# Optimization experiments

Measured on AMD Instinct MI355X. Metric: run time of the kernel, lower is better.

The kernel has to match this reference:

```python
import jax, jax.numpy as jnp
import numpy as np

L, D, N = 4096, 1024, 16  # seq_len, d_model, hiddens_per_input


def setup_inputs() -> dict:
    key = jax.random.key(0)
    ks = jax.random.split(key, 9)
    x = jax.random.normal(ks[0], (L, D), dtype=jnp.float32)
    # Delta param (pre-softplus); softplus(Delta) > 0 is the discretization step
    Delta = jax.random.normal(ks[1], (D,), dtype=jnp.float32)
    # A stored as (re, im); default scheme uses A_re = -1 (stable), theta in [0, 2pi)
    A_re = -(0.5 + 0.5 * jax.random.uniform(ks[2], (D, N), dtype=jnp.float32))
    A_im = jax.random.uniform(ks[3], (D, N), dtype=jnp.float32) * 2.0 * jnp.pi
    scale = 1.0 / jnp.sqrt(jnp.float32(D))  # matrix_init: randn / sqrt(shape[0])
    B_re = jax.random.normal(ks[4], (D, N), dtype=jnp.float32) * scale
    B_im = jax.random.normal(ks[5], (D, N), dtype=jnp.float32) * scale
    C_re = jax.random.normal(ks[6], (D, N), dtype=jnp.float32) * scale
    C_im = jax.random.normal(ks[7], (D, N), dtype=jnp.float32) * scale
    D_param = jax.random.normal(ks[8], (D,), dtype=jnp.float32) * scale
    return {"x": x, "Delta": Delta, "A_re": A_re, "A_im": A_im,
            "B_re": B_re, "B_im": B_im, "C_re": C_re, "C_im": C_im,
            "D_param": D_param}


def _binary_operator_diag(q_i, q_j):
    """Associative op for diagonal linear recurrence h_j = A_j h_{j-1} + b_j."""
    A_i, b_i = q_i
    A_j, b_j = q_j
    return (A_j * A_i, A_j * b_i + b_j)


def reference(x, Delta, A_re, A_im, B_re, B_im, C_re, C_im, D_param):
    Bc = B_re + 1j * B_im                      # (D, N) complex
    Cc = C_re + 1j * C_im                      # (D, N) complex
    Ac = A_re + 1j * A_im                      # (D, N) complex
    dt = jax.nn.softplus(Delta)                # (D,)
    # shared_Delta=True branch: Lambda = exp(dt[:, None] * A), repeated over L
    Lam = jnp.exp(dt[:, None] * Ac)            # (D, N) complex
    Lambda_elements = jnp.broadcast_to(Lam[None, :, :], (x.shape[0], *Lam.shape))
    # Bu = einsum('D, D N, L D -> L D N', dt, B, x)
    Bu_elements = jnp.einsum('D,DN,LD->LDN', dt.astype(Bc.dtype), Bc,
                             x.astype(Bc.dtype))
    _, hidden_states = jax.lax.associative_scan(
        _binary_operator_diag, (Lambda_elements, Bu_elements))  # (L, D, N)
    out = jnp.einsum('LDN,DN->LD', hidden_states, Cc) + D_param[None, :] * x
    return out.real
```

## Files before the change

kernel.cpp:

```cpp
#include <hip/hip_runtime.h>
#include <math.h>

constexpr int L  = 4096;
constexpr int D  = 1024;
constexpr int N  = 16;
constexpr int NC = 128;
constexpr int T  = L / NC;

__device__ __forceinline__ float softplus_f(float v) {
    return fmaxf(v, 0.0f) + log1pf(expf(-fabsf(v)));
}

__global__ __launch_bounds__(256) void k_pre(
    const float* __restrict__ Delta,
    const float* __restrict__ A_re, const float* __restrict__ A_im,
    const float* __restrict__ B_re, const float* __restrict__ B_im,
    const float* __restrict__ C_re, const float* __restrict__ C_im,
    float* __restrict__ PLr, float* __restrict__ PLi,
    float* __restrict__ PTr, float* __restrict__ PTi,
    float* __restrict__ PCr, float* __restrict__ PCi)
{
    const int tid = blockIdx.x * 256 + threadIdx.x;
    const int d = tid & (D - 1);
    const int n = tid >> 10;
    const int idx = d * N + n;

    const float dt = softplus_f(Delta[d]);
    float e  = expf(A_re[idx] * dt);
    float th = A_im[idx] * dt;
    float lr = e * cosf(th), li = e * sinf(th);
    float tr = lr, ti = li;
    #pragma unroll
    for (int k = 0; k < 5; ++k) {
        float nr = tr * tr - ti * ti;
        ti = 2.0f * tr * ti;
        tr = nr;
    }
    float br = B_re[idx], bi = B_im[idx];
    float cr = C_re[idx], ci = C_im[idx];
    PLr[tid] = lr; PLi[tid] = li;
    PTr[tid] = tr; PTi[tid] = ti;
    PCr[tid] = dt * (cr * br - ci * bi);
    PCi[tid] = dt * (cr * bi + ci * br);
}

__global__ __launch_bounds__(256, 4) void k_local(
    const float* __restrict__ x,
    const float* __restrict__ PLr, const float* __restrict__ PLi,
    float2* __restrict__ s2)
{
    __shared__ float xs[T * 64];
    const int bc = blockIdx.x >> 4;
    const int dg = blockIdx.x & 15;
    const int tid = threadIdx.x;

    const float* xg = x + (size_t)bc * T * D + dg * 64;
    #pragma unroll
    for (int it = 0; it < 2; ++it) {
        int f = tid * 4 + it * 1024;
        int row = f >> 6, col = f & 63;
        *(float4*)&xs[row * 64 + col] = *(const float4*)(xg + (size_t)row * D + col);
    }

    const int q = tid & 3, dl = tid >> 2;
    const int d = dg * 64 + dl;
    float Lr[4], Li[4];
    #pragma unroll
    for (int j = 0; j < 4; ++j) {
        int n = q * 4 + j;
        Lr[j] = PLr[n * D + d];
        Li[j] = PLi[n * D + d];
    }
    __syncthreads();

    float gr[4] = {0, 0, 0, 0}, gi[4] = {0, 0, 0, 0};
    #pragma unroll
    for (int i = 0; i < T; ++i) {
        float xv = xs[i * 64 + dl];
        #pragma unroll
        for (int j = 0; j < 4; ++j) {
            float t2 = fmaf(-Li[j], gi[j], xv);
            float nr = fmaf(Lr[j], gr[j], t2);
            gi[j] = fmaf(Lr[j], gi[j], Li[j] * gr[j]);
            gr[j] = nr;
        }
    }
    #pragma unroll
    for (int j = 0; j < 4; ++j) {
        int n = q * 4 + j;
        s2[((size_t)bc * N + n) * D + d] = make_float2(gr[j], gi[j]);
    }
}

__global__ __launch_bounds__(256) void k_scan(
    const float* __restrict__ PTr, const float* __restrict__ PTi,
    float2* __restrict__ s2)
{
    const int tid = blockIdx.x * 256 + threadIdx.x;
    const float Lr = PTr[tid], Li = PTi[tid];

    float cr = 0.0f, ci = 0.0f;
    for (int c0 = 0; c0 < NC; c0 += 16) {
        float2 sv[16];
        #pragma unroll
        for (int u = 0; u < 16; ++u)
            sv[u] = s2[(size_t)(c0 + u) * (N * D) + tid];
        #pragma unroll
        for (int u = 0; u < 16; ++u) {
            s2[(size_t)(c0 + u) * (N * D) + tid] = make_float2(cr, ci);
            float nr = fmaf(Lr, cr, fmaf(-Li, ci, sv[u].x));
            ci = fmaf(Lr, ci, fmaf(Li, cr, sv[u].y));
            cr = nr;
        }
    }
}

__global__ __launch_bounds__(256, 4) void k_out(
    const float* __restrict__ x,
    const float* __restrict__ PLr, const float* __restrict__ PLi,
    const float* __restrict__ PCr, const float* __restrict__ PCi,
    const float* __restrict__ Dp,
    const float2* __restrict__ s2,
    float* __restrict__ out)
{
    __shared__ float xs[T * 64];
    const int bc = blockIdx.x >> 4;
    const int dg = blockIdx.x & 15;
    const int tid = threadIdx.x;

    const float* xg = x + (size_t)bc * T * D + dg * 64;
    #pragma unroll
    for (int it = 0; it < 2; ++it) {
        int f = tid * 4 + it * 1024;
        int row = f >> 6, col = f & 63;
        *(float4*)&xs[row * 64 + col] = *(const float4*)(xg + (size_t)row * D + col);
    }

    const int q = tid & 3, dl = tid >> 2;
    const int d = dg * 64 + dl;
    float Lr[4], Li[4], Cr[4], Ci[4], gr[4], gi[4];
    #pragma unroll
    for (int j = 0; j < 4; ++j) {
        int n = q * 4 + j;
        Lr[j] = PLr[n * D + d];
        Li[j] = PLi[n * D + d];
        Cr[j] = PCr[n * D + d];
        Ci[j] = PCi[n * D + d];
        float2 cv = s2[((size_t)bc * N + n) * D + d];
        gr[j] = cv.x; gi[j] = cv.y;
    }
    const float dpv = Dp[d];
    float* og = out + (size_t)bc * T * D + dg * 64;
    __syncthreads();

    #pragma unroll
    for (int ib = 0; ib < T / 4; ++ib) {
        float keep = 0.0f;
        #pragma unroll
        for (int u = 0; u < 4; ++u) {
            int i = ib * 4 + u;
            float xv = xs[i * 64 + dl];
            float acc = 0.0f;
            #pragma unroll
            for (int j = 0; j < 4; ++j) {
                float t2 = fmaf(-Li[j], gi[j], xv);
                float nr = fmaf(Lr[j], gr[j], t2);
                gi[j] = fmaf(Lr[j], gi[j], Li[j] * gr[j]);
                gr[j] = nr;
                acc = fmaf(Cr[j], gr[j], acc);
                acc = fmaf(-Ci[j], gi[j], acc);
            }
            acc += __shfl_xor(acc, 1);
            acc += __shfl_xor(acc, 2);
            acc = fmaf(dpv, xv, acc);
            keep = (q == u) ? acc : keep;
        }
        og[(size_t)(ib * 4 + q) * D + dl] = keep;
    }
}

extern "C" void kernel_launch(void* const* d_in, const int* in_sizes, int n_in,
                              void* d_out, int out_size, void* d_ws, size_t ws_size,
                              hipStream_t stream) {
    const float* x     = (const float*)d_in[0];
    const float* Delta = (const float*)d_in[1];
    const float* A_re  = (const float*)d_in[2];
    const float* A_im  = (const float*)d_in[3];
    const float* B_re  = (const float*)d_in[4];
    const float* B_im  = (const float*)d_in[5];
    const float* C_re  = (const float*)d_in[6];
    const float* C_im  = (const float*)d_in[7];
    const float* Dp    = (const float*)d_in[8];
    float* out = (float*)d_out;

    float2* s2 = (float2*)d_ws;
    float* pbase = (float*)((char*)d_ws + (size_t)NC * N * D * sizeof(float2));
    float* PLr = pbase + 0 * (N * D);
    float* PLi = pbase + 1 * (N * D);
    float* PTr = pbase + 2 * (N * D);
    float* PTi = pbase + 3 * (N * D);
    float* PCr = pbase + 4 * (N * D);
    float* PCi = pbase + 5 * (N * D);

    k_pre<<<(N * D) / 256, 256, 0, stream>>>(Delta, A_re, A_im, B_re, B_im,
                                             C_re, C_im, PLr, PLi, PTr, PTi,
                                             PCr, PCi);
    k_local<<<NC * (D / 64), 256, 0, stream>>>(x, PLr, PLi, s2);
    k_scan<<<(N * D) / 256, 256, 0, stream>>>(PTr, PTi, s2);
    k_out<<<NC * (D / 64), 256, 0, stream>>>(x, PLr, PLi, PCr, PCi, Dp, s2, out);
}
```

Before: 117.5 us.

## Fuse chunked SSM scan into one cooperative kernel with grid syncs

Result: slower. 336.8 us (+186.7%).

```diff
diff --git a/kernel.cpp b/kernel.cpp
--- a/kernel.cpp
+++ b/kernel.cpp
@@ -1,15 +1,162 @@
 #include <hip/hip_runtime.h>
+#include <hip/hip_cooperative_groups.h>
 #include <math.h>
 
-constexpr int L  = 4096;
-constexpr int D  = 1024;
-constexpr int N  = 16;
-constexpr int NC = 128;
-constexpr int T  = L / NC;
+namespace cg = cooperative_groups;
+
+constexpr int L = 4096;
+constexpr int D = 1024;
+constexpr int N = 16;
+
+constexpr int FNC = 64;
+constexpr int FT  = L / FNC;
+constexpr int FG  = 16;
+constexpr int FDG = D / FG;
+constexpr int FNB = FNC * FG;
 
 __device__ __forceinline__ float softplus_f(float v) {
     return fmaxf(v, 0.0f) + log1pf(expf(-fabsf(v)));
 }
+
+__global__ __launch_bounds__(256, 4) void k_fused(
+    const float* __restrict__ x, const float* __restrict__ Delta,
+    const float* __restrict__ A_re, const float* __restrict__ A_im,
+    const float* __restrict__ B_re, const float* __restrict__ B_im,
+    const float* __restrict__ C_re, const float* __restrict__ C_im,
+    const float* __restrict__ Dp, float* __restrict__ out,
+    float2* __restrict__ s2)
+{
+    cg::grid_group grid = cg::this_grid();
+    __shared__ float xs[FT * FDG];
+    const int b  = blockIdx.x;
+    const int c  = b >> 4;
+    const int dg = b & 15;
+    const int t  = threadIdx.x;
+
+    const float* xg = x + (size_t)c * FT * D + dg * FDG;
+    #pragma unroll
+    for (int it = 0; it < 4; ++it) {
+        int f = t * 4 + it * 1024;
+        int row = f >> 6, col = f & 63;
+        *(float4*)&xs[row * FDG + col] =
+            *(const float4*)(xg + (size_t)row * D + col);
+    }
+
+    const int q = t & 3, dl = t >> 2;
+    const int d = dg * FDG + dl;
+    const float dt  = softplus_f(Delta[d]);
+    float Lr[4], Li[4], Cr[4], Ci[4];
+    {
+        const int pidx = d * N + q * 4;
+        float4 a0 = *(const float4*)(A_re + pidx);
+        float4 a1 = *(const float4*)(A_im + pidx);
+        float4 b0 = *(const float4*)(B_re + pidx);
+        float4 b1 = *(const float4*)(B_im + pidx);
+        float4 c0 = *(const float4*)(C_re + pidx);
+        float4 c1 = *(const float4*)(C_im + pidx);
+        const float ar[4] = {a0.x, a0.y, a0.z, a0.w};
+        const float ai[4] = {a1.x, a1.y, a1.z, a1.w};
+        const float br[4] = {b0.x, b0.y, b0.z, b0.w};
+        const float bi[4] = {b1.x, b1.y, b1.z, b1.w};
+        const float cr[4] = {c0.x, c0.y, c0.z, c0.w};
+        const float ci[4] = {c1.x, c1.y, c1.z, c1.w};
+        #pragma unroll
+        for (int j = 0; j < 4; ++j) {
+            float e  = expf(ar[j] * dt);
+            float th = ai[j] * dt;
+            Lr[j] = e * cosf(th);
+            Li[j] = e * sinf(th);
+            Cr[j] = dt * (cr[j] * br[j] - ci[j] * bi[j]);
+            Ci[j] = dt * (cr[j] * bi[j] + ci[j] * br[j]);
+        }
+    }
+    __syncthreads();
+
+    float gr[4] = {0, 0, 0, 0}, gi[4] = {0, 0, 0, 0};
+    #pragma unroll
+    for (int i = 0; i < FT; ++i) {
+        float xv = xs[i * FDG + dl];
+        #pragma unroll
+        for (int j = 0; j < 4; ++j) {
+            float t2 = fmaf(-Li[j], gi[j], xv);
+            float nr = fmaf(Lr[j], gr[j], t2);
+            gi[j] = fmaf(Lr[j], gi[j], Li[j] * gr[j]);
+            gr[j] = nr;
+        }
+    }
+    #pragma unroll
+    for (int j = 0; j < 4; ++j)
+        s2[((size_t)c * N + q * 4 + j) * D + d] = make_float2(gr[j], gi[j]);
+
+    grid.sync();
+
+    const int pid = b * 256 + t;
+    if (pid < N * D) {
+        const int pd = pid & (D - 1);
+        const int pn = pid >> 10;
+        const float pdt = softplus_f(Delta[pd]);
+        float e  = expf(A_re[pd * N + pn] * pdt);
+        float th = A_im[pd * N + pn] * pdt;
+        float lr = e * cosf(th), li = e * sinf(th);
+        #pragma unroll
+        for (int k = 0; k < 6; ++k) {
+            float nr = lr * lr - li * li;
+            li = 2.0f * lr * li;
+            lr = nr;
+        }
+        float cr = 0.0f, ci = 0.0f;
+        for (int c0 = 0; c0 < FNC; c0 += 8) {
+            float2 sv[8];
+            #pragma unroll
+            for (int u = 0; u < 8; ++u)
+                sv[u] = s2[((size_t)(c0 + u) * N + pn) * D + pd];
+            #pragma unroll
+            for (int u = 0; u < 8; ++u) {
+                s2[((size_t)(c0 + u) * N + pn) * D + pd] = make_float2(cr, ci);
+                float nr = fmaf(lr, cr, fmaf(-li, ci, sv[u].x));
+                ci = fmaf(lr, ci, fmaf(li, cr, sv[u].y));
+                cr = nr;
+            }
+        }
+    }
+
+    grid.sync();
+
+    #pragma unroll
+    for (int j = 0; j < 4; ++j) {
+        float2 cv = s2[((size_t)c * N + q * 4 + j) * D + d];
+        gr[j] = cv.x; gi[j] = cv.y;
+    }
+    const float dpv = Dp[d];
+    float* og = out + (size_t)c * FT * D + dg * FDG;
+    #pragma unroll
+    for (int ib = 0; ib < FT / 4; ++ib) {
+        float keep = 0.0f;
+        #pragma unroll
+        for (int u = 0; u < 4; ++u) {
+            int i = ib * 4 + u;
+            float xv = xs[i * FDG + dl];
+            float acc = 0.0f;
+            #pragma unroll
+            for (int j = 0; j < 4; ++j) {
+                float t2 = fmaf(-Li[j], gi[j], xv);
+                float nr = fmaf(Lr[j], gr[j], t2);
+                gi[j] = fmaf(Lr[j], gi[j], Li[j] * gr[j]);
+                gr[j] = nr;
+                acc = fmaf(Cr[j], gr[j], acc);
+                acc = fmaf(-Ci[j], gi[j], acc);
+            }
+            acc += __shfl_xor(acc, 1);
+            acc += __shfl_xor(acc, 2);
+            acc = fmaf(dpv, xv, acc);
+            keep = (q == u) ? acc : keep;
+        }
+        og[(size_t)(ib * 4 + q) * D + dl] = keep;
+    }
+}
+
+constexpr int BNC = 128;
+constexpr int BT  = L / BNC;
 
 __global__ __launch_bounds__(256) void k_pre(
     const float* __restrict__ Delta,
@@ -24,7 +171,6 @@
     const int d = tid & (D - 1);
     const int n = tid >> 10;
     const int idx = d * N + n;
-
     const float dt = softplus_f(Delta[d]);
     float e  = expf(A_re[idx] * dt);
     float th = A_im[idx] * dt;
@@ -49,19 +195,17 @@
     const float* __restrict__ PLr, const float* __restrict__ PLi,
     float2* __restrict__ s2)
 {
-    __shared__ float xs[T * 64];
+    __shared__ float xs[BT * 64];
     const int bc = blockIdx.x >> 4;
     const int dg = blockIdx.x & 15;
     const int tid = threadIdx.x;
-
-    const float* xg = x + (size_t)bc * T * D + dg * 64;
+    const float* xg = x + (size_t)bc * BT * D + dg * 64;
     #pragma unroll
     for (int it = 0; it < 2; ++it) {
         int f = tid * 4 + it * 1024;
         int row = f >> 6, col = f & 63;
         *(float4*)&xs[row * 64 + col] = *(const float4*)(xg + (size_t)row * D + col);
     }
-
     const int q = tid & 3, dl = tid >> 2;
     const int d = dg * 64 + dl;
     float Lr[4], Li[4];
@@ -72,10 +216,9 @@
         Li[j] = PLi[n * D + d];
     }
     __syncthreads();
-
     float gr[4] = {0, 0, 0, 0}, gi[4] = {0, 0, 0, 0};
     #pragma unroll
-    for (int i = 0; i < T; ++i) {
+    for (int i = 0; i < BT; ++i) {
         float xv = xs[i * 64 + dl];
         #pragma unroll
         for (int j = 0; j < 4; ++j) {
@@ -98,9 +241,8 @@
 {
     const int tid = blockIdx.x * 256 + threadIdx.x;
     const float Lr = PTr[tid], Li = PTi[tid];
-
     float cr = 0.0f, ci = 0.0f;
-    for (int c0 = 0; c0 < NC; c0 += 16) {
+    for (int c0 = 0; c0 < BNC; c0 += 16) {
         float2 sv[16];
         #pragma unroll
         for (int u = 0; u < 16; ++u)
@@ -123,19 +265,17 @@
     const float2* __restrict__ s2,
     float* __restrict__ out)
 {
-    __shared__ float xs[T * 64];
+    __shared__ float xs[BT * 64];
     const int bc = blockIdx.x >> 4;
     const int dg = blockIdx.x & 15;
     const int tid = threadIdx.x;
-
-    const float* xg = x + (size_t)bc * T * D + dg * 64;
+    const float* xg = x + (size_t)bc * BT * D + dg * 64;
     #pragma unroll
     for (int it = 0; it < 2; ++it) {
         int f = tid * 4 + it * 1024;
         int row = f >> 6, col = f & 63;
         *(float4*)&xs[row * 64 + col] = *(const float4*)(xg + (size_t)row * D + col);
     }
-
     const int q = tid & 3, dl = tid >> 2;
     const int d = dg * 64 + dl;
     float Lr[4], Li[4], Cr[4], Ci[4], gr[4], gi[4];
@@ -150,11 +290,10 @@
         gr[j] = cv.x; gi[j] = cv.y;
     }
     const float dpv = Dp[d];
-    float* og = out + (size_t)bc * T * D + dg * 64;
+    float* og = out + (size_t)bc * BT * D + dg * 64;
     __syncthreads();
-
-    #pragma unroll
-    for (int ib = 0; ib < T / 4; ++ib) {
+    #pragma unroll
+    for (int ib = 0; ib < BT / 4; ++ib) {
         float keep = 0.0f;
         #pragma unroll
         for (int u = 0; u < 4; ++u) {
@@ -192,20 +331,28 @@
     const float* C_im  = (const float*)d_in[7];
     const float* Dp    = (const float*)d_in[8];
     float* out = (float*)d_out;
-
     float2* s2 = (float2*)d_ws;
-    float* pbase = (float*)((char*)d_ws + (size_t)NC * N * D * sizeof(float2));
-    float* PLr = pbase + 0 * (N * D);
-    float* PLi = pbase + 1 * (N * D);
-    float* PTr = pbase + 2 * (N * D);
-    float* PTi = pbase + 3 * (N * D);
-    float* PCr = pbase + 4 * (N * D);
-    float* PCi = pbase + 5 * (N * D);
-
-    k_pre<<<(N * D) / 256, 256, 0, stream>>>(Delta, A_re, A_im, B_re, B_im,
-                                             C_re, C_im, PLr, PLi, PTr, PTi,
-                                             PCr, PCi);
-    k_local<<<NC * (D / 64), 256, 0, stream>>>(x, PLr, PLi, s2);
-    k_scan<<<(N * D) / 256, 256, 0, stream>>>(PTr, PTi, s2);
-    k_out<<<NC * (D / 64), 256, 0, stream>>>(x, PLr, PLi, PCr, PCi, Dp, s2, out);
-}
+
+    void* args[] = {(void*)&x, (void*)&Delta, (void*)&A_re, (void*)&A_im,
+                    (void*)&B_re, (void*)&B_im, (void*)&C_re, (void*)&C_im,
+                    (void*)&Dp, (void*)&out, (void*)&s2};
+    hipError_t err = hipLaunchCooperativeKernel((const void*)k_fused,
+                                                dim3(FNB), dim3(256),
+                                                args, 0, stream);
+    if (err != hipSuccess) {
+        float* pbase = (float*)((char*)d_ws + (size_t)BNC * N * D * sizeof(float2));
+        float* PLr = pbase + 0 * (N * D);
+        float* PLi = pbase + 1 * (N * D);
+        float* PTr = pbase + 2 * (N * D);
+        float* PTi = pbase + 3 * (N * D);
+        float* PCr = pbase + 4 * (N * D);
+        float* PCi = pbase + 5 * (N * D);
+        k_pre<<<(N * D) / 256, 256, 0, stream>>>(Delta, A_re, A_im, B_re, B_im,
+                                                 C_re, C_im, PLr, PLi, PTr, PTi,
+                                                 PCr, PCi);
+        k_local<<<BNC * (D / 64), 256, 0, stream>>>(x, PLr, PLi, s2);
+        k_scan<<<(N * D) / 256, 256, 0, stream>>>(PTr, PTi, s2);
+        k_out<<<BNC * (D / 64), 256, 0, stream>>>(x, PLr, PLi, PCr, PCi, Dp,
+                                                  s2, out);
+    }
+}
```

## Fuse parameter precompute into scan kernels and halve chunk count

Applied to the files above, without the earlier changes.

After: 111.3 us. 1.06x faster.

```diff
diff --git a/kernel.cpp b/kernel.cpp
--- a/kernel.cpp
+++ b/kernel.cpp
@@ -4,79 +4,62 @@
 constexpr int L  = 4096;
 constexpr int D  = 1024;
 constexpr int N  = 16;
-constexpr int NC = 128;
+constexpr int NC = 64;
 constexpr int T  = L / NC;
+constexpr int DG = 64;
+constexpr int G  = D / DG;
 
 __device__ __forceinline__ float softplus_f(float v) {
     return fmaxf(v, 0.0f) + log1pf(expf(-fabsf(v)));
 }
 
-__global__ __launch_bounds__(256) void k_pre(
+__device__ __forceinline__ void lam_fast(float ar, float ai, float dt,
+                                         float& lr, float& li) {
+    float e = __expf(ar * dt);
+    float s, c;
+    __sincosf(ai * dt, &s, &c);
+    lr = e * c;
+    li = e * s;
+}
+
+__global__ __launch_bounds__(256, 4) void k_local(
+    const float* __restrict__ x,
     const float* __restrict__ Delta,
     const float* __restrict__ A_re, const float* __restrict__ A_im,
-    const float* __restrict__ B_re, const float* __restrict__ B_im,
-    const float* __restrict__ C_re, const float* __restrict__ C_im,
-    float* __restrict__ PLr, float* __restrict__ PLi,
-    float* __restrict__ PTr, float* __restrict__ PTi,
-    float* __restrict__ PCr, float* __restrict__ PCi)
-{
-    const int tid = blockIdx.x * 256 + threadIdx.x;
-    const int d = tid & (D - 1);
-    const int n = tid >> 10;
-    const int idx = d * N + n;
-
-    const float dt = softplus_f(Delta[d]);
-    float e  = expf(A_re[idx] * dt);
-    float th = A_im[idx] * dt;
-    float lr = e * cosf(th), li = e * sinf(th);
-    float tr = lr, ti = li;
-    #pragma unroll
-    for (int k = 0; k < 5; ++k) {
-        float nr = tr * tr - ti * ti;
-        ti = 2.0f * tr * ti;
-        tr = nr;
-    }
-    float br = B_re[idx], bi = B_im[idx];
-    float cr = C_re[idx], ci = C_im[idx];
-    PLr[tid] = lr; PLi[tid] = li;
-    PTr[tid] = tr; PTi[tid] = ti;
-    PCr[tid] = dt * (cr * br - ci * bi);
-    PCi[tid] = dt * (cr * bi + ci * br);
-}
-
-__global__ __launch_bounds__(256, 4) void k_local(
-    const float* __restrict__ x,
-    const float* __restrict__ PLr, const float* __restrict__ PLi,
     float2* __restrict__ s2)
 {
-    __shared__ float xs[T * 64];
-    const int bc = blockIdx.x >> 4;
+    __shared__ float xs[T * DG];
+    const int c  = blockIdx.x >> 4;
     const int dg = blockIdx.x & 15;
-    const int tid = threadIdx.x;
-
-    const float* xg = x + (size_t)bc * T * D + dg * 64;
-    #pragma unroll
-    for (int it = 0; it < 2; ++it) {
-        int f = tid * 4 + it * 1024;
+    const int t  = threadIdx.x;
+
+    const float* xg = x + (size_t)c * T * D + dg * DG;
+    #pragma unroll
+    for (int it = 0; it < 4; ++it) {
+        int f = t * 4 + it * 1024;
         int row = f >> 6, col = f & 63;
-        *(float4*)&xs[row * 64 + col] = *(const float4*)(xg + (size_t)row * D + col);
-    }
-
-    const int q = tid & 3, dl = tid >> 2;
-    const int d = dg * 64 + dl;
+        *(float4*)&xs[row * DG + col] =
+            *(const float4*)(xg + (size_t)row * D + col);
+    }
+
+    const int q = t & 3, dl = t >> 2;
+    const int d = dg * DG + dl;
+    const float dt = softplus_f(Delta[d]);
     float Lr[4], Li[4];
-    #pragma unroll
-    for (int j = 0; j < 4; ++j) {
-        int n = q * 4 + j;
-        Lr[j] = PLr[n * D + d];
-        Li[j] = PLi[n * D + d];
+    {
+        float4 a0 = *(const float4*)(A_re + d * N + q * 4);
+        float4 a1 = *(const float4*)(A_im + d * N + q * 4);
+        const float ar[4] = {a0.x, a0.y, a0.z, a0.w};
+        const float ai[4] = {a1.x, a1.y, a1.z, a1.w};
+        #pragma unroll
+        for (int j = 0; j < 4; ++j) lam_fast(ar[j], ai[j], dt, Lr[j], Li[j]);
     }
     __syncthreads();
 
     float gr[4] = {0, 0, 0, 0}, gi[4] = {0, 0, 0, 0};
     #pragma unroll
     for (int i = 0; i < T; ++i) {
-        float xv = xs[i * 64 + dl];
+        float xv = xs[i * DG + dl];
         #pragma unroll
         for (int j = 0; j < 4; ++j) {
             float t2 = fmaf(-Li[j], gi[j], xv);
@@ -86,20 +69,31 @@
         }
     }
     #pragma unroll
-    for (int j = 0; j < 4; ++j) {
-        int n = q * 4 + j;
-        s2[((size_t)bc * N + n) * D + d] = make_float2(gr[j], gi[j]);
-    }
+    for (int j = 0; j < 4; ++j)
+        s2[((size_t)c * N + q * 4 + j) * D + d] = make_float2(gr[j], gi[j]);
 }
 
 __global__ __launch_bounds__(256) void k_scan(
-    const float* __restrict__ PTr, const float* __restrict__ PTi,
+    const float* __restrict__ Delta,
+    const float* __restrict__ A_re, const float* __restrict__ A_im,
     float2* __restrict__ s2)
 {
     const int tid = blockIdx.x * 256 + threadIdx.x;
-    const float Lr = PTr[tid], Li = PTi[tid];
+    const int d = tid & (D - 1);
+    const int n = tid >> 10;
+
+    const float dt = softplus_f(Delta[d]);
+    float Lr, Li;
+    lam_fast(A_re[d * N + n], A_im[d * N + n], dt, Lr, Li);
+    #pragma unroll
+    for (int k = 0; k < 6; ++k) {
+        float nr = Lr * Lr - Li * Li;
+        Li = 2.0f * Lr * Li;
+        Lr = nr;
+    }
 
     float cr = 0.0f, ci = 0.0f;
+    #pragma unroll
     for (int c0 = 0; c0 < NC; c0 += 16) {
         float2 sv[16];
         #pragma unroll
@@ -117,40 +111,61 @@
 
 __global__ __launch_bounds__(256, 4) void k_out(
     const float* __restrict__ x,
-    const float* __restrict__ PLr, const float* __restrict__ PLi,
-    const float* __restrict__ PCr, const float* __restrict__ PCi,
+    const float* __restrict__ Delta,
+    const float* __restrict__ A_re, const float* __restrict__ A_im,
+    const float* __restrict__ B_re, const float* __restrict__ B_im,
+    const float* __restrict__ C_re, const float* __restrict__ C_im,
     const float* __restrict__ Dp,
     const float2* __restrict__ s2,
     float* __restrict__ out)
 {
-    __shared__ float xs[T * 64];
-    const int bc = blockIdx.x >> 4;
+    __shared__ float xs[T * DG];
+    const int c  = blockIdx.x >> 4;
     const int dg = blockIdx.x & 15;
-    const int tid = threadIdx.x;
-
-    const float* xg = x + (size_t)bc * T * D + dg * 64;
-    #pragma unroll
-    for (int it = 0; it < 2; ++it) {
-        int f = tid * 4 + it * 1024;
+    const int t  = threadIdx.x;
+
+    const float* xg = x + (size_t)c * T * D + dg * DG;
+    #pragma unroll
+    for (int it = 0; it < 4; ++it) {
+        int f = t * 4 + it * 1024;
         int row = f >> 6, col = f & 63;
-        *(float4*)&xs[row * 64 + col] = *(const float4*)(xg + (size_t)row * D + col);
-    }
-
-    const int q = tid & 3, dl = tid >> 2;
-    const int d = dg * 64 + dl;
+        *(float4*)&xs[row * DG + col] =
+            *(const float4*)(xg + (size_t)row * D + col);
+    }
+
+    const int q = t & 3, dl = t >> 2;
+    const int d = dg * DG + dl;
+    const float dt  = softplus_f(Delta[d]);
+    const float dpv = Dp[d];
+
     float Lr[4], Li[4], Cr[4], Ci[4], gr[4], gi[4];
+    {
+        const int pidx = d * N + q * 4;
+        float4 a0 = *(const float4*)(A_re + pidx);
+        float4 a1 = *(const float4*)(A_im + pidx);
+        float4 b0 = *(const float4*)(B_re + pidx);
+        float4 b1 = *(const float4*)(B_im + pidx);
+        float4 c0 = *(const float4*)(C_re + pidx);
+        float4 c1 = *(const float4*)(C_im + pidx);
+        const float ar[4] = {a0.x, a0.y, a0.z, a0.w};
+        const float ai[4] = {a1.x, a1.y, a1.z, a1.w};
+        const float br[4] = {b0.x, b0.y, b0.z, b0.w};
+        const float bi[4] = {b1.x, b1.y, b1.z, b1.w};
+        const float crr[4] = {c0.x, c0.y, c0.z, c0.w};
+        const float cii[4] = {c1.x, c1.y, c1.z, c1.w};
+        #pragma unroll
+        for (int j = 0; j < 4; ++j) {
+            lam_fast(ar[j], ai[j], dt, Lr[j], Li[j]);
+            Cr[j] = dt * (crr[j] * br[j] - cii[j] * bi[j]);
+            Ci[j] = dt * (crr[j] * bi[j] + cii[j] * br[j]);
+        }
+    }
     #pragma unroll
     for (int j = 0; j < 4; ++j) {
-        int n = q * 4 + j;
-        Lr[j] = PLr[n * D + d];
-        Li[j] = PLi[n * D + d];
-        Cr[j] = PCr[n * D + d];
-        Ci[j] = PCi[n * D + d];
-        float2 cv = s2[((size_t)bc * N + n) * D + d];
+        float2 cv = s2[((size_t)c * N + q * 4 + j) * D + d];
         gr[j] = cv.x; gi[j] = cv.y;
     }
-    const float dpv = Dp[d];
-    float* og = out + (size_t)bc * T * D + dg * 64;
+    float* og = out + (size_t)c * T * D + dg * DG;
     __syncthreads();
 
     #pragma unroll
@@ -159,7 +174,7 @@
         #pragma unroll
         for (int u = 0; u < 4; ++u) {
             int i = ib * 4 + u;
-            float xv = xs[i * 64 + dl];
+            float xv = xs[i * DG + dl];
             float acc = 0.0f;
             #pragma unroll
             for (int j = 0; j < 4; ++j) {
@@ -192,20 +207,10 @@
     const float* C_im  = (const float*)d_in[7];
     const float* Dp    = (const float*)d_in[8];
     float* out = (float*)d_out;
-
     float2* s2 = (float2*)d_ws;
-    float* pbase = (float*)((char*)d_ws + (size_t)NC * N * D * sizeof(float2));
-    float* PLr = pbase + 0 * (N * D);
-    float* PLi = pbase + 1 * (N * D);
-    float* PTr = pbase + 2 * (N * D);
-    float* PTi = pbase + 3 * (N * D);
-    float* PCr = pbase + 4 * (N * D);
-    float* PCi = pbase + 5 * (N * D);
-
-    k_pre<<<(N * D) / 256, 256, 0, stream>>>(Delta, A_re, A_im, B_re, B_im,
-                                             C_re, C_im, PLr, PLi, PTr, PTi,
-                                             PCr, PCi);
-    k_local<<<NC * (D / 64), 256, 0, stream>>>(x, PLr, PLi, s2);
-    k_scan<<<(N * D) / 256, 256, 0, stream>>>(PTr, PTi, s2);
-    k_out<<<NC * (D / 64), 256, 0, stream>>>(x, PLr, PLi, PCr, PCi, Dp, s2, out);
-}
+
+    k_local<<<NC * G, 256, 0, stream>>>(x, Delta, A_re, A_im, s2);
+    k_scan<<<(N * D) / 256, 256, 0, stream>>>(Delta, A_re, A_im, s2);
+    k_out<<<NC * G, 256, 0, stream>>>(x, Delta, A_re, A_im, B_re, B_im,
+                                      C_re, C_im, Dp, s2, out);
+}
```
